# Optimization experiments

Measured on AMD Instinct MI355X. Metric: run time of the kernel, lower is better.

Reference implementation:

```python
import jax, jax.numpy as jnp
import numpy as np

N_NODES = 50000
EPS = 1e-12  # F.normalize eps


def sage_conv(x, src, dst, W_l, b_l, W_r):
    # PyG SAGEConv: out = lin_l(mean_j x_j) + lin_r(x_i), then L2 normalize.
    n = x.shape[0]
    agg = jax.ops.segment_sum(x[src], dst, num_segments=n)          # [N, d]
    cnt = jax.ops.segment_sum(jnp.ones_like(src, dtype=x.dtype), dst,
                              num_segments=n)                       # [N]
    mean = agg / jnp.maximum(cnt, 1.0)[:, None]
    out = mean @ W_l.T + b_l + x @ W_r.T
    norm = jnp.linalg.norm(out, axis=-1, keepdims=True)
    return out / jnp.maximum(norm, EPS)


def setup_inputs() -> dict:
    key = jax.random.key(0)
    ks = jax.random.split(key, 8)
    nfeat, nhid, nclass = 64, 64, 10
    E = 1250000
    features = jax.random.normal(ks[0], (N_NODES, nfeat), dtype=jnp.float32)
    edge_index = jax.random.randint(ks[1], (2, E), 0, N_NODES, dtype=jnp.int64)
    s1 = 1.0 / np.sqrt(nfeat)
    s2 = 1.0 / np.sqrt(nhid)
    return {
        "features": features,
        "edge_index": edge_index,
        "W1_l": jax.random.normal(ks[2], (nhid, nfeat), dtype=jnp.float32) * s1,
        "b1": jnp.zeros((nhid,), dtype=jnp.float32),
        "W1_r": jax.random.normal(ks[3], (nhid, nfeat), dtype=jnp.float32) * s1,
        "W2_l": jax.random.normal(ks[4], (nclass, nhid), dtype=jnp.float32) * s2,
        "b2": jnp.zeros((nclass,), dtype=jnp.float32),
        "W2_r": jax.random.normal(ks[5], (nclass, nhid), dtype=jnp.float32) * s2,
    }


def reference(features, edge_index, W1_l, b1, W1_r, W2_l, b2, W2_r):
    src, dst = edge_index[0], edge_index[1]
    x = jax.nn.relu(sage_conv(features, src, dst, W1_l, b1, W1_r))
    # dropout is identity in eval mode
    x = sage_conv(x, src, dst, W2_l, b2, W2_r)
    return jax.nn.log_softmax(x, axis=1)
```

## Files before the change

kernel.cpp:

```cpp
#include <hip/hip_runtime.h>
#include <hip/hip_bf16.h>


static constexpr int FEAT = 64;
static constexpr int SLOTS = 64;
static constexpr int BUCK_SZ = 6250;

__device__ __forceinline__ unsigned short f2bf(float f) {
  __hip_bfloat16 h = __float2bfloat16(f);
  return *reinterpret_cast<unsigned short*>(&h);
}
__device__ __forceinline__ unsigned int pk2(float a, float b) {
  return (unsigned)f2bf(a) | ((unsigned)f2bf(b) << 16);
}
__device__ __forceinline__ float bfl(unsigned int u) {
  return __uint_as_float(u << 16);
}
__device__ __forceinline__ float bfh(unsigned int u) {
  return __uint_as_float(u & 0xFFFF0000u);
}
__device__ __forceinline__ void acc8(float* a, const uint4& w) {
  a[0] += bfl(w.x); a[1] += bfh(w.x); a[2] += bfl(w.y); a[3] += bfh(w.y);
  a[4] += bfl(w.z); a[5] += bfh(w.z); a[6] += bfl(w.w); a[7] += bfh(w.w);
}

__global__ __launch_bounds__(256) void dense1_kernel(
    const float* __restrict__ x,
    const float* __restrict__ Wl, const float* __restrict__ Wr,
    const float* __restrict__ b,
    unsigned short* __restrict__ p, float* __restrict__ q,
    int* __restrict__ cursor, uint4* __restrict__ p2, int N) {
  __shared__ float4 Ws[16 * 16];
  int mat = blockIdx.y >> 2;
  int og = blockIdx.y & 3;
  const float4* Wg = (const float4*)(mat ? Wr : Wl);
  int tid = threadIdx.x;
  Ws[tid] = Wg[(og * 16) * 16 + tid];

  int node = blockIdx.x * 256 + tid;
  if (blockIdx.y == 0 && node < N) cursor[node] = 0;
  __syncthreads();
  if (node >= N) {
    if (node == N && blockIdx.y == 0) {
      uint4 z = make_uint4(0u, 0u, 0u, 0u);
      uint4* z1 = (uint4*)(p + (size_t)N * 64);
#pragma unroll
      for (int r = 0; r < 8; ++r) z1[r] = z;
      p2[(size_t)N * 2] = z;
      p2[(size_t)N * 2 + 1] = z;
    }
    return;
  }

  const float4* X4 = (const float4*)x + (size_t)node * 16;
  float4 xr[16];
#pragma unroll
  for (int kq = 0; kq < 16; ++kq) xr[kq] = X4[kq];

  float acc[16];
#pragma unroll 4
  for (int o = 0; o < 16; ++o) {
    float a = 0.0f;
#pragma unroll
    for (int kq = 0; kq < 16; ++kq) {
      float4 w = Ws[o * 16 + kq];
      float4 xv = xr[kq];
      a = fmaf(xv.x, w.x, fmaf(xv.y, w.y, fmaf(xv.z, w.z, fmaf(xv.w, w.w, a))));
    }
    acc[o] = a;
  }

  if (mat) {
    float4* O4 = (float4*)(q + (size_t)node * FEAT + og * 16);
    const float4* B4 = (const float4*)(b + og * 16);
#pragma unroll
    for (int oq = 0; oq < 4; ++oq) {
      float4 bv = B4[oq];
      O4[oq] = make_float4(acc[oq * 4] + bv.x, acc[oq * 4 + 1] + bv.y,
                           acc[oq * 4 + 2] + bv.z, acc[oq * 4 + 3] + bv.w);
    }
  } else {
    uint4 w0, w1;
    w0.x = pk2(acc[0], acc[1]);
    w0.y = pk2(acc[2], acc[3]);
    w0.z = pk2(acc[4], acc[5]);
    w0.w = pk2(acc[6], acc[7]);
    w1.x = pk2(acc[8], acc[9]);
    w1.y = pk2(acc[10], acc[11]);
    w1.z = pk2(acc[12], acc[13]);
    w1.w = pk2(acc[14], acc[15]);
    uint4* O = (uint4*)p + (size_t)node * 8 + og * 2;
    O[0] = w0;
    O[1] = w1;
  }
}

__global__ __launch_bounds__(256) void fill_kernel(
    const int* __restrict__ src, const int* __restrict__ dst,
    int* __restrict__ cursor, unsigned short* __restrict__ col, int E) {
  int b = blockIdx.x & 7;
  int e = (blockIdx.x >> 3) * 256 + threadIdx.x;
  if (e >= E) return;
  int d = __builtin_nontemporal_load(dst + e);
  int lo = b * BUCK_SZ;
  if (d >= lo && d < lo + BUCK_SZ) {
    int s = __builtin_nontemporal_load(src + e);
    int pos = atomicAdd(&cursor[d], 1);
    if (pos < SLOTS) col[d * SLOTS + pos] = (unsigned short)s;
  }
}

__global__ __launch_bounds__(256) void gather1_dense2_kernel(
    const int* __restrict__ cursor, const unsigned short* __restrict__ col,
    const uint4* __restrict__ p1, const float* __restrict__ q1,
    const float* __restrict__ W2l, const float* __restrict__ W2r,
    const float* __restrict__ b2,
    uint4* __restrict__ p2, float* __restrict__ q2, int N) {
  __shared__ float4 Wall[2 * 10 * 17];
  __shared__ float bs[10];
  int tid = threadIdx.x;
  if (tid < 160) {
    int c = tid >> 4, k = tid & 15;
    Wall[c * 17 + k] = ((const float4*)W2l)[tid];
    Wall[170 + c * 17 + k] = ((const float4*)W2r)[tid];
  }
  if (tid < 10) bs[tid] = b2[tid];
  __syncthreads();

  int wave = tid >> 6, lane = tid & 63;
  int g = lane >> 3, q = lane & 7;
  int node = blockIdx.x * 4 + wave;
  if (node >= N) return;

  int deg = cursor[node];
  int cnt = min(deg, SLOTS);
  int beg = node * SLOTS;
  int cv = (int)col[beg + lane];

  float a[8];
#pragma unroll
  for (int j = 0; j < 8; ++j) a[j] = 0.0f;

  {
    int t0 = __shfl(cv, g), t1 = __shfl(cv, 8 + g);
    int t2 = __shfl(cv, 16 + g), t3 = __shfl(cv, 24 + g);
    int s0 = (g < cnt) ? t0 : N;
    int s1 = (8 + g < cnt) ? t1 : N;
    int s2 = (16 + g < cnt) ? t2 : N;
    int s3 = (24 + g < cnt) ? t3 : N;
    uint4 w0 = p1[(size_t)s0 * 8 + q];
    uint4 w1 = p1[(size_t)s1 * 8 + q];
    uint4 w2 = p1[(size_t)s2 * 8 + q];
    uint4 w3 = p1[(size_t)s3 * 8 + q];
    acc8(a, w0); acc8(a, w1); acc8(a, w2); acc8(a, w3);
  }
  if (cnt > 32) {
    int t0 = __shfl(cv, 32 + g), t1 = __shfl(cv, 40 + g);
    int t2 = __shfl(cv, 48 + g), t3 = __shfl(cv, 56 + g);
    int s0 = (32 + g < cnt) ? t0 : N;
    int s1 = (40 + g < cnt) ? t1 : N;
    int s2 = (48 + g < cnt) ? t2 : N;
    int s3 = (56 + g < cnt) ? t3 : N;
    uint4 w0 = p1[(size_t)s0 * 8 + q];
    uint4 w1 = p1[(size_t)s1 * 8 + q];
    uint4 w2 = p1[(size_t)s2 * 8 + q];
    uint4 w3 = p1[(size_t)s3 * 8 + q];
    acc8(a, w0); acc8(a, w1); acc8(a, w2); acc8(a, w3);
  }

#pragma unroll
  for (int off = 8; off <= 32; off <<= 1) {
#pragma unroll
    for (int j = 0; j < 8; ++j) a[j] += __shfl_xor(a[j], off);
  }

  float invc = 1.0f / (float)max(deg, 1);
  const float4* Q4 = (const float4*)q1 + (size_t)node * 16 + q * 2;
  float4 q0 = Q4[0], q1v = Q4[1];
  float v[8];
  v[0] = fmaf(a[0], invc, q0.x); v[1] = fmaf(a[1], invc, q0.y);
  v[2] = fmaf(a[2], invc, q0.z); v[3] = fmaf(a[3], invc, q0.w);
  v[4] = fmaf(a[4], invc, q1v.x); v[5] = fmaf(a[5], invc, q1v.y);
  v[6] = fmaf(a[6], invc, q1v.z); v[7] = fmaf(a[7], invc, q1v.w);

  float ss = 0.0f;
#pragma unroll
  for (int j = 0; j < 8; ++j) ss += v[j] * v[j];
#pragma unroll
  for (int off = 1; off <= 4; off <<= 1) ss += __shfl_xor(ss, off);
  float scale = 1.0f / fmaxf(sqrtf(ss), 1e-12f);

  float h[8];
#pragma unroll
  for (int j = 0; j < 8; ++j) h[j] = fmaxf(v[j] * scale, 0.0f);

  float res[3];
#pragma unroll
  for (int r = 0; r < 3; ++r) {
    int t = r * 8 + g;
    int base = (t < 10) ? 0 : 170;
    int c = (t < 10) ? t : (t - 10);
    c = min(c, 9);
    float4 wa = Wall[base + c * 17 + q * 2];
    float4 wb = Wall[base + c * 17 + q * 2 + 1];
    float pr = fmaf(h[0], wa.x, fmaf(h[1], wa.y, fmaf(h[2], wa.z,
               fmaf(h[3], wa.w, fmaf(h[4], wb.x, fmaf(h[5], wb.y,
               fmaf(h[6], wb.z, h[7] * wb.w)))))));
    pr += __shfl_xor(pr, 1);
    pr += __shfl_xor(pr, 2);
    pr += __shfl_xor(pr, 4);
    res[r] = pr;
  }

  float pv[10], qv[10];
#pragma unroll
  for (int i = 0; i < 10; ++i) {
    pv[i] = __shfl(res[i >> 3], (i & 7) * 8);
    int t2 = 10 + i;
    qv[i] = __shfl(res[t2 >> 3], (t2 & 7) * 8);
  }

  if (lane == 0) {
    uint4 w0, w1;
    w0.x = pk2(pv[0], pv[1]); w0.y = pk2(pv[2], pv[3]);
    w0.z = pk2(pv[4], pv[5]); w0.w = pk2(pv[6], pv[7]);
    w1.x = pk2(pv[8], pv[9]); w1.y = 0u; w1.z = 0u; w1.w = 0u;
    p2[(size_t)node * 2] = w0;
    p2[(size_t)node * 2 + 1] = w1;
  } else if (lane == 1) {
    *(float4*)(q2 + (size_t)node * 16) =
        make_float4(qv[0] + bs[0], qv[1] + bs[1], qv[2] + bs[2], qv[3] + bs[3]);
  } else if (lane == 2) {
    *(float4*)(q2 + (size_t)node * 16 + 4) =
        make_float4(qv[4] + bs[4], qv[5] + bs[5], qv[6] + bs[6], qv[7] + bs[7]);
  } else if (lane == 3) {
    *(float4*)(q2 + (size_t)node * 16 + 8) =
        make_float4(qv[8] + bs[8], qv[9] + bs[9], 0.f, 0.f);
  } else if (lane == 4) {
    *(float4*)(q2 + (size_t)node * 16 + 12) = make_float4(0.f, 0.f, 0.f, 0.f);
  }
}

__global__ __launch_bounds__(256) void gather2_kernel(
    const int* __restrict__ cursor, const unsigned short* __restrict__ col,
    const uint4* __restrict__ p2, const float* __restrict__ q2,
    float* __restrict__ out, int N) {
  int tid = threadIdx.x;
  int wave = tid >> 6, lane = tid & 63;
  int g = lane >> 1, q = lane & 1;
  int node = blockIdx.x * 4 + wave;
  if (node >= N) return;

  int deg = cursor[node];
  int cnt = min(deg, SLOTS);
  int beg = node * SLOTS;
  int cv = (int)col[beg + lane];

  float a[8];
#pragma unroll
  for (int j = 0; j < 8; ++j) a[j] = 0.0f;

  {
    int t0 = __shfl(cv, g);
    int s0 = (g < cnt) ? t0 : N;
    uint4 w0 = p2[(size_t)s0 * 2 + q];
    acc8(a, w0);
  }
  if (cnt > 32) {
    int t1 = __shfl(cv, 32 + g);
    int s1 = (32 + g < cnt) ? t1 : N;
    uint4 w1 = p2[(size_t)s1 * 2 + q];
    acc8(a, w1);
  }

#pragma unroll
  for (int off = 2; off <= 32; off <<= 1) {
#pragma unroll
    for (int j = 0; j < 8; ++j) a[j] += __shfl_xor(a[j], off);
  }

  float invc = 1.0f / (float)max(deg, 1);
  const float4* Q4 = (const float4*)q2 + (size_t)node * 4 + q * 2;
  float4 q0 = Q4[0], q1 = Q4[1];
  float v[8];
  v[0] = fmaf(a[0], invc, q0.x); v[1] = fmaf(a[1], invc, q0.y);
  v[2] = fmaf(a[2], invc, q0.z); v[3] = fmaf(a[3], invc, q0.w);
  v[4] = fmaf(a[4], invc, q1.x); v[5] = fmaf(a[5], invc, q1.y);
  v[6] = fmaf(a[6], invc, q1.z); v[7] = fmaf(a[7], invc, q1.w);

  float ss = 0.0f;
#pragma unroll
  for (int j = 0; j < 8; ++j) ss += v[j] * v[j];
  ss += __shfl_xor(ss, 1);
  float scale = 1.0f / fmaxf(sqrtf(ss), 1e-12f);
#pragma unroll
  for (int j = 0; j < 8; ++j) v[j] *= scale;

  float m;
  if (q == 0) {
    m = v[0];
#pragma unroll
    for (int j = 1; j < 8; ++j) m = fmaxf(m, v[j]);
  } else {
    m = fmaxf(v[0], v[1]);
  }
  m = fmaxf(m, __shfl_xor(m, 1));

  float es = 0.0f;
  if (q == 0) {
#pragma unroll
    for (int j = 0; j < 8; ++j) es += __expf(v[j] - m);
  } else {
    es = __expf(v[0] - m) + __expf(v[1] - m);
  }
  es += __shfl_xor(es, 1);
  float lse = m + __logf(es);

  if (g == 0) {
    float2* o = (float2*)(out + (size_t)node * 10);
    if (q == 0) {
      o[0] = make_float2(v[0] - lse, v[1] - lse);
      o[1] = make_float2(v[2] - lse, v[3] - lse);
      o[2] = make_float2(v[4] - lse, v[5] - lse);
      o[3] = make_float2(v[6] - lse, v[7] - lse);
    } else {
      o[4] = make_float2(v[0] - lse, v[1] - lse);
    }
  }
}

extern "C" void kernel_launch(void* const* d_in, const int* in_sizes, int n_in,
                              void* d_out, int out_size, void* d_ws, size_t ws_size,
                              hipStream_t stream) {
  const float* features = (const float*)d_in[0];
  const int* edge_index = (const int*)d_in[1];
  const float* W1_l = (const float*)d_in[2];
  const float* b1   = (const float*)d_in[3];
  const float* W1_r = (const float*)d_in[4];
  const float* W2_l = (const float*)d_in[5];
  const float* b2   = (const float*)d_in[6];
  const float* W2_r = (const float*)d_in[7];
  float* out = (float*)d_out;

  const int N = in_sizes[0] / FEAT;
  const int E = in_sizes[1] / 2;
  const int* src = edge_index;
  const int* dst = edge_index + E;

  char* ws = (char*)d_ws;
  int* cursor            = (int*)(ws + 0);
  unsigned short* col    = (unsigned short*)(ws + 200064);
  unsigned short* p1     = (unsigned short*)(ws + 6600064);
  float* q1              = (float*)(ws + 13000192);
  uint4* p2              = (uint4*)(ws + 25800192);
  float* q2              = (float*)(ws + 27400256);

  int eb8 = ((E + 255) / 256) * 8;
  int nb256 = (N + 255) / 256;
  int nbw = (N + 3) / 4;

  dense1_kernel<<<dim3(nb256, 8), 256, 0, stream>>>(
      features, W1_l, W1_r, b1, p1, q1, cursor, p2, N);
  fill_kernel<<<eb8, 256, 0, stream>>>(src, dst, cursor, col, E);
  gather1_dense2_kernel<<<nbw, 256, 0, stream>>>(
      cursor, col, (const uint4*)p1, q1, W2_l, W2_r, b2, p2, q2, N);
  gather2_kernel<<<nbw, 256, 0, stream>>>(
      cursor, col, (const uint4*)p2, q2, out, N);
}
```

Before: 225.0 us.

## Loop output groups in dense1, split fill into two launches, hoist q loads

dense1 now launches 2 grid rows instead of 8. Each thread loads its x row once and loops over all four 16-wide output groups, with the full 64x64 weight matrix held in shared memory. This removes four redundant reads of x per matrix but gives the grid fewer, longer blocks. fill_kernel is split into two launches, each covering half the edge range. The q1/q2 residual loads in both gather kernels are moved before the neighbor gather so their latency overlaps it.

```diff
diff --git a/kernel.cpp b/kernel.cpp
--- a/kernel.cpp
+++ b/kernel.cpp
@@ -29,25 +29,25 @@
     const float* __restrict__ Wl, const float* __restrict__ Wr,
     const float* __restrict__ b,
     unsigned short* __restrict__ p, float* __restrict__ q,
-    int* __restrict__ cursor, uint4* __restrict__ p2, int N) {
-  __shared__ float4 Ws[16 * 16];
-  int mat = blockIdx.y >> 2;
-  int og = blockIdx.y & 3;
+    int* __restrict__ cursor, uint4* __restrict__ p2z, int N) {
+  __shared__ float4 Ws[64 * 16];
+  int mat = blockIdx.y;
   const float4* Wg = (const float4*)(mat ? Wr : Wl);
   int tid = threadIdx.x;
-  Ws[tid] = Wg[(og * 16) * 16 + tid];
+#pragma unroll
+  for (int i = 0; i < 4; ++i) Ws[i * 256 + tid] = Wg[i * 256 + tid];
 
   int node = blockIdx.x * 256 + tid;
-  if (blockIdx.y == 0 && node < N) cursor[node] = 0;
+  if (mat == 0 && node < N) cursor[node] = 0;
   __syncthreads();
   if (node >= N) {
-    if (node == N && blockIdx.y == 0) {
+    if (node == N && mat == 0) {
       uint4 z = make_uint4(0u, 0u, 0u, 0u);
       uint4* z1 = (uint4*)(p + (size_t)N * 64);
 #pragma unroll
       for (int r = 0; r < 8; ++r) z1[r] = z;
-      p2[(size_t)N * 2] = z;
-      p2[(size_t)N * 2 + 1] = z;
+      p2z[(size_t)N * 2] = z;
+      p2z[(size_t)N * 2 + 1] = z;
     }
     return;
   }
@@ -57,50 +57,54 @@
 #pragma unroll
   for (int kq = 0; kq < 16; ++kq) xr[kq] = X4[kq];
 
-  float acc[16];
+#pragma unroll 1
+  for (int og = 0; og < 4; ++og) {
+    float acc[16];
 #pragma unroll 4
-  for (int o = 0; o < 16; ++o) {
-    float a = 0.0f;
-#pragma unroll
-    for (int kq = 0; kq < 16; ++kq) {
-      float4 w = Ws[o * 16 + kq];
-      float4 xv = xr[kq];
-      a = fmaf(xv.x, w.x, fmaf(xv.y, w.y, fmaf(xv.z, w.z, fmaf(xv.w, w.w, a))));
+    for (int o = 0; o < 16; ++o) {
+      float a = 0.0f;
+#pragma unroll
+      for (int kq = 0; kq < 16; ++kq) {
+        float4 w = Ws[(og * 16 + o) * 16 + kq];
+        float4 xv = xr[kq];
+        a = fmaf(xv.x, w.x, fmaf(xv.y, w.y, fmaf(xv.z, w.z, fmaf(xv.w, w.w, a))));
+      }
+      acc[o] = a;
     }
-    acc[o] = a;
-  }
-
-  if (mat) {
-    float4* O4 = (float4*)(q + (size_t)node * FEAT + og * 16);
-    const float4* B4 = (const float4*)(b + og * 16);
-#pragma unroll
-    for (int oq = 0; oq < 4; ++oq) {
-      float4 bv = B4[oq];
-      O4[oq] = make_float4(acc[oq * 4] + bv.x, acc[oq * 4 + 1] + bv.y,
-                           acc[oq * 4 + 2] + bv.z, acc[oq * 4 + 3] + bv.w);
+
+    if (mat) {
+      float4* O4 = (float4*)(q + (size_t)node * FEAT + og * 16);
+      const float4* B4 = (const float4*)(b + og * 16);
+#pragma unroll
+      for (int oq = 0; oq < 4; ++oq) {
+        float4 bv = B4[oq];
+        O4[oq] = make_float4(acc[oq * 4] + bv.x, acc[oq * 4 + 1] + bv.y,
+                             acc[oq * 4 + 2] + bv.z, acc[oq * 4 + 3] + bv.w);
+      }
+    } else {
+      uint4 w0, w1;
+      w0.x = pk2(acc[0], acc[1]);
+      w0.y = pk2(acc[2], acc[3]);
+      w0.z = pk2(acc[4], acc[5]);
+      w0.w = pk2(acc[6], acc[7]);
+      w1.x = pk2(acc[8], acc[9]);
+      w1.y = pk2(acc[10], acc[11]);
+      w1.z = pk2(acc[12], acc[13]);
+      w1.w = pk2(acc[14], acc[15]);
+      uint4* O = (uint4*)p + (size_t)node * 8 + og * 2;
+      O[0] = w0;
+      O[1] = w1;
     }
-  } else {
-    uint4 w0, w1;
-    w0.x = pk2(acc[0], acc[1]);
-    w0.y = pk2(acc[2], acc[3]);
-    w0.z = pk2(acc[4], acc[5]);
-    w0.w = pk2(acc[6], acc[7]);
-    w1.x = pk2(acc[8], acc[9]);
-    w1.y = pk2(acc[10], acc[11]);
-    w1.z = pk2(acc[12], acc[13]);
-    w1.w = pk2(acc[14], acc[15]);
-    uint4* O = (uint4*)p + (size_t)node * 8 + og * 2;
-    O[0] = w0;
-    O[1] = w1;
   }
 }
 
 __global__ __launch_bounds__(256) void fill_kernel(
     const int* __restrict__ src, const int* __restrict__ dst,
-    int* __restrict__ cursor, unsigned short* __restrict__ col, int E) {
+    int* __restrict__ cursor, unsigned short* __restrict__ col,
+    int e0, int e1) {
   int b = blockIdx.x & 7;
-  int e = (blockIdx.x >> 3) * 256 + threadIdx.x;
-  if (e >= E) return;
+  int e = e0 + (blockIdx.x >> 3) * 256 + threadIdx.x;
+  if (e >= e1) return;
   int d = __builtin_nontemporal_load(dst + e);
   int lo = b * BUCK_SZ;
   if (d >= lo && d < lo + BUCK_SZ) {
@@ -137,6 +141,9 @@
   int beg = node * SLOTS;
   int cv = (int)col[beg + lane];
 
+  const float4* Q4 = (const float4*)q1 + (size_t)node * 16 + q * 2;
+  float4 q0 = Q4[0], q1v = Q4[1];
+
   float a[8];
 #pragma unroll
   for (int j = 0; j < 8; ++j) a[j] = 0.0f;
@@ -175,8 +182,6 @@
   }
 
   float invc = 1.0f / (float)max(deg, 1);
-  const float4* Q4 = (const float4*)q1 + (size_t)node * 16 + q * 2;
-  float4 q0 = Q4[0], q1v = Q4[1];
   float v[8];
   v[0] = fmaf(a[0], invc, q0.x); v[1] = fmaf(a[1], invc, q0.y);
   v[2] = fmaf(a[2], invc, q0.z); v[3] = fmaf(a[3], invc, q0.w);
@@ -256,6 +261,9 @@
   int beg = node * SLOTS;
   int cv = (int)col[beg + lane];
 
+  const float4* Q4 = (const float4*)q2 + (size_t)node * 4 + q * 2;
+  float4 q0 = Q4[0], q1 = Q4[1];
+
   float a[8];
 #pragma unroll
   for (int j = 0; j < 8; ++j) a[j] = 0.0f;
@@ -280,8 +288,6 @@
   }
 
   float invc = 1.0f / (float)max(deg, 1);
-  const float4* Q4 = (const float4*)q2 + (size_t)node * 4 + q * 2;
-  float4 q0 = Q4[0], q1 = Q4[1];
   float v[8];
   v[0] = fmaf(a[0], invc, q0.x); v[1] = fmaf(a[1], invc, q0.y);
   v[2] = fmaf(a[2], invc, q0.z); v[3] = fmaf(a[3], invc, q0.w);
@@ -355,13 +361,15 @@
   uint4* p2              = (uint4*)(ws + 25800192);
   float* q2              = (float*)(ws + 27400256);
 
-  int eb8 = ((E + 255) / 256) * 8;
+  int Eh = E / 2;
+  int ebh = ((Eh + 255) / 256) * 8;
   int nb256 = (N + 255) / 256;
   int nbw = (N + 3) / 4;
 
-  dense1_kernel<<<dim3(nb256, 8), 256, 0, stream>>>(
+  dense1_kernel<<<dim3(nb256, 2), 256, 0, stream>>>(
       features, W1_l, W1_r, b1, p1, q1, cursor, p2, N);
-  fill_kernel<<<eb8, 256, 0, stream>>>(src, dst, cursor, col, E);
+  fill_kernel<<<ebh, 256, 0, stream>>>(src, dst, cursor, col, 0, Eh);
+  fill_kernel<<<ebh, 256, 0, stream>>>(src, dst, cursor, col, Eh, E);
   gather1_dense2_kernel<<<nbw, 256, 0, stream>>>(
       cursor, col, (const uint4*)p1, q1, W2_l, W2_r, b2, p2, q2, N);
   gather2_kernel<<<nbw, 256, 0, stream>>>(
```

New measurement: 235.3 us. +4.6%, slower.
